# Kernel optimization log

Measured on AMD Instinct MI355X. Metric: run time of the kernel, lower is better.

The kernel has to match this reference:

```python
import jax, jax.numpy as jnp
import numpy as np

B, C, H, W, K = 64, 64, 32, 32, 1024  # C == dim_dict, K == size_dict
BETA = 0.25


def setup_inputs() -> dict:
    key = jax.random.key(0)
    k1, k2, k3 = jax.random.split(key, 3)
    return {
        "z_from_encoder": jax.random.normal(k1, (B, C, H, W), dtype=jnp.float32),
        "codebook": jax.random.normal(k2, (K, C), dtype=jnp.float32),
        "codebook_weight": jax.random.normal(k3, (K,), dtype=jnp.float32),
        "flg_train": 1,
    }


def reference(z_from_encoder, codebook, codebook_weight, flg_train):
    # NCHW -> NHWC, flatten to (N, D)
    z = jnp.transpose(z_from_encoder, (0, 2, 3, 1))
    zf = z.reshape(-1, z.shape[-1])                      # (N, D)
    # squared euclidean distances via expansion (N, K)
    d = (jnp.sum(zf ** 2, axis=1, keepdims=True)
         + jnp.sum(codebook ** 2, axis=1)
         - 2.0 * zf @ codebook.T)
    idx = jnp.argmin(d, axis=1)                          # (N,)
    # one-hot @ codebook == gather
    z_q = codebook[idx].reshape(z.shape)                 # (B, H, W, D)
    if flg_train:
        loss = (BETA * jnp.mean((jax.lax.stop_gradient(z_q) - z) ** 2)
                + jnp.mean((z_q - jax.lax.stop_gradient(z)) ** 2))
    else:
        loss = jnp.float32(0.0)
    # straight-through estimator
    z_q_st = z + jax.lax.stop_gradient(z_q - z)
    # codebook usage histogram -> perplexity
    n_tok = zf.shape[0]
    e_mean = jnp.zeros((codebook.shape[0],), z.dtype).at[idx].add(1.0) / n_tok
    perplexity = jnp.exp(-jnp.sum(e_mean * jnp.log(e_mean + 1e-10)))
    z_q_out = jnp.transpose(z_q_st, (0, 3, 1, 2))        # back to NCHW
    return z_q_out, loss, perplexity
```

## Files before the change

kernel.cpp:

```cpp
#include <hip/hip_runtime.h>


typedef __attribute__((ext_vector_type(8))) short short8;
typedef __attribute__((ext_vector_type(4))) float float4v;

#define NELEM 4194304

#define WS_CBF   0
#define WS_C2H   262144
#define WS_HIST  266240
#define WS_LOSS  270336
#define WS_IDX   270592

__device__ __forceinline__ unsigned bf16_rne(float x) {
    unsigned u = __float_as_uint(x);
    return (u + 0x7fffu + ((u >> 16) & 1u)) >> 16;
}


__global__ __launch_bounds__(256) void prep_kernel(
    const float* __restrict__ z, const float* __restrict__ cb,
    ushort* __restrict__ zs, ushort* __restrict__ cbf, float* __restrict__ c2h,
    int* __restrict__ hist, float* __restrict__ loss_part)
{
    __shared__ float s_c2[2][16];
    int tid  = threadIdx.x;
    int lane = tid & 63, wave = tid >> 6;
    int quad = lane >> 4, col = lane & 15;
    int bx   = blockIdx.x;

    if (bx < 1024) {
        int tokbase = bx * 64;
        int bb = tokbase >> 10, hwb = tokbase & 1023;
        const float* zb = z + bb * 65536 + hwb;
        int g  = wave;
        int gg = bx * 4 + g;
        int rel = g * 16 + col;
#pragma unroll
        for (int st = 0; st < 2; st++) {
            short8 h8, l8;
#pragma unroll
            for (int j = 0; j < 8; j++) {
                int d = st * 32 + quad * 8 + j;
                float x = zb[d * 1024 + rel];
                unsigned hb = bf16_rne(x);
                h8[j] = (short)hb;
                l8[j] = (short)bf16_rne(x - __uint_as_float(hb << 16));
            }
            int base = (((gg * 2 + st) * 4 + quad) * 2 + 0) * 16 + col;
            *(short8*)(zs + base * 8)             = h8;
            *(short8*)(zs + (base + 16) * 8)      = l8;
        }
        return;
    }
    if (bx >= 1088) {
        hist[(bx - 1088) * 256 + tid] = 0;
        if (bx == 1088 && tid < 64) loss_part[tid] = 0.f;
        return;
    }
    int c = bx - 1024, fid = wave;
    int st = fid & 1, split = fid >> 1;
    int code  = c * 16 + col;
    int dbase = st * 32 + quad * 8;
    const float* cp = cb + code * 64 + dbase;
    float4v v0 = *(const float4v*)cp;
    float4v v1 = *(const float4v*)(cp + 4);
    float xs[8] = {v0.x, v0.y, v0.z, v0.w, v1.x, v1.y, v1.z, v1.w};
    short8 frag;
    float ssq = 0.f;
#pragma unroll
    for (int j = 0; j < 8; j++) {
        float x = xs[j];
        ssq = fmaf(x, x, ssq);
        unsigned hb = bf16_rne(x);
        if (split == 0) frag[j] = (short)hb;
        else            frag[j] = (short)bf16_rne(x - __uint_as_float(hb << 16));
    }
    *(short8*)(cbf + ((c * 4 + fid) * 64 + lane) * 8) = frag;
    if (split == 0) {
        ssq += __shfl_xor(ssq, 16);
        ssq += __shfl_xor(ssq, 32);
        if (quad == 0) s_c2[st][col] = ssq;
    }
    __syncthreads();
    if (tid < 16) c2h[c * 16 + tid] = -0.5f * (s_c2[0][tid] + s_c2[1][tid]);
}

__global__ __launch_bounds__(256, 3) void argmin_kernel(
    const ushort* __restrict__ zs, const ushort* __restrict__ cbf,
    const float* __restrict__ c2h, int* __restrict__ idx_out, int* __restrict__ hist)
{
    __shared__ float s_ms[4][64];
    __shared__ int   s_mi[4][64];

    int tid  = threadIdx.x;
    int lane = tid & 63, wave = tid >> 6;
    int quad = lane >> 4, col = lane & 15;
    int bx   = blockIdx.x;
    int tokbase = bx * 64;

    short8 ah[4][2], al[4][2];
#pragma unroll
    for (int g = 0; g < 4; g++) {
        int gg = bx * 4 + g;
#pragma unroll
        for (int st = 0; st < 2; st++) {
            int base = (((gg * 2 + st) * 4 + quad) * 2 + 0) * 16 + col;
            ah[g][st] = *(const short8*)(zs + base * 8);
            al[g][st] = *(const short8*)(zs + (base + 16) * 8);
        }
    }

    float best[4][4]; int bidx[4][4];
#pragma unroll
    for (int g = 0; g < 4; g++)
#pragma unroll
        for (int r = 0; r < 4; r++) { best[g][r] = -1e38f; bidx[g][r] = 0; }

    int cbase = wave << 4;
    const ushort* cw = cbf + lane * 8;
    {
        const ushort* p0 = cw + cbase * 2048;
        short8 nb0 = *(const short8*)(p0 + 0);
        short8 nb1 = *(const short8*)(p0 + 512);
        short8 nb2 = *(const short8*)(p0 + 1024);
        short8 nb3 = *(const short8*)(p0 + 1536);
        float  nini = c2h[cbase * 16 + col];
        for (int cc = 0; cc < 16; cc++) {
            short8 bh0 = nb0, bh1 = nb1, bl0 = nb2, bl1 = nb3;
            float  ini = nini;
            if (cc < 15) {
                const ushort* np = cw + (cbase + cc + 1) * 2048;
                nb0 = *(const short8*)(np + 0);
                nb1 = *(const short8*)(np + 512);
                nb2 = *(const short8*)(np + 1024);
                nb3 = *(const short8*)(np + 1536);
                nini = c2h[(cbase + cc + 1) * 16 + col];
            }
            int code = (cbase + cc) * 16 + col;
#pragma unroll
            for (int g = 0; g < 4; g++) {
                float4v acc = {ini, ini, ini, ini};
                acc = __builtin_amdgcn_mfma_f32_16x16x32_bf16(ah[g][0], bh0, acc, 0, 0, 0);
                acc = __builtin_amdgcn_mfma_f32_16x16x32_bf16(ah[g][1], bh1, acc, 0, 0, 0);
                acc = __builtin_amdgcn_mfma_f32_16x16x32_bf16(ah[g][0], bl0, acc, 0, 0, 0);
                acc = __builtin_amdgcn_mfma_f32_16x16x32_bf16(ah[g][1], bl1, acc, 0, 0, 0);
                acc = __builtin_amdgcn_mfma_f32_16x16x32_bf16(al[g][0], bh0, acc, 0, 0, 0);
                acc = __builtin_amdgcn_mfma_f32_16x16x32_bf16(al[g][1], bh1, acc, 0, 0, 0);
#pragma unroll
                for (int r = 0; r < 4; r++) {
                    if (acc[r] > best[g][r]) { best[g][r] = acc[r]; bidx[g][r] = code; }
                }
            }
        }
    }

#pragma unroll
    for (int g = 0; g < 4; g++) {
#pragma unroll
        for (int r = 0; r < 4; r++) {
            float s = best[g][r]; int ix = bidx[g][r];
#pragma unroll
            for (int m = 1; m <= 8; m <<= 1) {
                float so = __shfl_xor(s, m);
                int   io = __shfl_xor(ix, m);
                if (so > s || (so == s && io < ix)) { s = so; ix = io; }
            }
            if (col == 0) {
                int t = g * 16 + quad * 4 + r;
                s_ms[wave][t] = s; s_mi[wave][t] = ix;
            }
        }
    }
    __syncthreads();

    if (tid < 64) {
        float sb = s_ms[0][tid]; int ib = s_mi[0][tid];
#pragma unroll
        for (int q = 1; q < 4; q++) {
            float sq_ = s_ms[q][tid];
            if (sq_ > sb) { sb = sq_; ib = s_mi[q][tid]; }
        }
        idx_out[tokbase + tid] = ib;
        atomicAdd(&hist[ib], 1);
    }
}

__global__ __launch_bounds__(256) void output_kernel(
    const float* __restrict__ z, const float* __restrict__ cb,
    const int* __restrict__ idx, float* __restrict__ out,
    float* __restrict__ loss_part)
{
    __shared__ int    s_row[128];
    __shared__ float4 s_q4[64 * 33];
    __shared__ float  s_red[4];

    int tid = threadIdx.x, bx = blockIdx.x;
    int tokbase = bx * 128;
    int bb = tokbase >> 10, hwb = tokbase & 1023;

    if (tid < 128) s_row[tid] = idx[tokbase + tid];
    __syncthreads();

#pragma unroll
    for (int p = 0; p < 32; p++) {
        int i = p * 256 + tid;
        int t = i >> 6, d = i & 63;
        float v = cb[s_row[t] * 64 + d];
        ((float*)s_q4)[(d * 33 + (t >> 2)) * 4 + (t & 3)] = v;
    }
    __syncthreads();

    const float* zb = z   + bb * 65536 + hwb;
    float*       ob = out + bb * 65536 + hwb;
    float ls = 0.f;
#pragma unroll
    for (int p = 0; p < 8; p++) {
        int fi = p * 256 + tid;
        int d = fi >> 5, tq = fi & 31;
        float4 zv = *(const float4*)(zb + d * 1024 + tq * 4);
        float4 qv = s_q4[d * 33 + tq];
        float d0 = qv.x - zv.x, d1 = qv.y - zv.y, d2 = qv.z - zv.z, d3 = qv.w - zv.w;
        float4 ov = {zv.x + d0, zv.y + d1, zv.z + d2, zv.w + d3};
        *(float4*)(ob + d * 1024 + tq * 4) = ov;
        ls += (d0 * d0 + d1 * d1) + (d2 * d2 + d3 * d3);
    }
#pragma unroll
    for (int off = 32; off; off >>= 1) ls += __shfl_down(ls, off);
    if ((tid & 63) == 0) s_red[tid >> 6] = ls;
    __syncthreads();
    if (tid == 0) {
        float v = (s_red[0] + s_red[1]) + (s_red[2] + s_red[3]);
        atomicAdd(&loss_part[bx & 63], v);
    }
}

__global__ __launch_bounds__(1024) void finalize_kernel(
    const int* __restrict__ hist, const float* __restrict__ loss_part,
    const int* __restrict__ flg, float* __restrict__ out) {
    __shared__ float red[16];
    int   k = threadIdx.x;
    float e = (float)hist[k] * (1.0f / 65536.0f);
    float v = e * logf(e + 1e-10f);
#pragma unroll
    for (int off = 32; off; off >>= 1) v += __shfl_down(v, off);
    if ((k & 63) == 0) red[k >> 6] = v;
    __syncthreads();
    if (k == 0) {
        float s = 0.f;
#pragma unroll
        for (int i = 0; i < 16; i++) s += red[i];
        out[NELEM + 1] = expf(-s);

        float ls = 0.f;
        for (int i = 0; i < 64; i++) ls += loss_part[i];
        float m    = ls * (1.0f / (float)NELEM);
        out[NELEM] = (*flg) ? (0.25f * m + m) : 0.0f;
    }
}

extern "C" void kernel_launch(void* const* d_in, const int* in_sizes, int n_in,
                              void* d_out, int out_size, void* d_ws, size_t ws_size,
                              hipStream_t stream) {
    const float* z   = (const float*)d_in[0];
    const float* cb  = (const float*)d_in[1];
    const int*   flg = (const int*)d_in[3];

    float* out = (float*)d_out;
    char*  ws  = (char*)d_ws;

    ushort* cbf       = (ushort*)(ws + WS_CBF);
    float*  c2h       = (float*)(ws + WS_C2H);
    int*    hist      = (int*)(ws + WS_HIST);
    float*  loss_part = (float*)(ws + WS_LOSS);
    int*    idx       = (int*)(ws + WS_IDX);
    ushort* zs        = (ushort*)d_out;

    prep_kernel<<<1092, 256, 0, stream>>>(z, cb, zs, cbf, c2h, hist, loss_part);
    argmin_kernel<<<1024, 256, 0, stream>>>(zs, cbf, c2h, idx, hist);
    output_kernel<<<512, 256, 0, stream>>>(z, cb, idx, out, loss_part);
    finalize_kernel<<<1, 1024, 0, stream>>>(hist, loss_part, flg, out);
}
```

Baseline: 135.6 us.

## Stage codebook chunks in LDS via async loads shared across waves

The argmin kernel is restructured. Each block now has 8 waves, each owning 16 tokens and sweeping all 64 codebook chunks. Before, each of 4 waves owned 64 tokens and a quarter of the codebook. Codebook fragments are double-buffered in LDS through global_load_lds by 4 waves and shared across all 8 waves, and c2h is cached in shared memory. This removes the cross-wave reduction and cuts per-wave register pressure. In exchange it adds a __syncthreads per chunk and does less MFMA work per B-fragment load.

```diff
diff --git a/kernel.cpp b/kernel.cpp
--- a/kernel.cpp
+++ b/kernel.cpp
@@ -15,6 +15,12 @@
 __device__ __forceinline__ unsigned bf16_rne(float x) {
     unsigned u = __float_as_uint(x);
     return (u + 0x7fffu + ((u >> 16) & 1u)) >> 16;
+}
+
+__device__ __forceinline__ void gl_lds16(const void* g, void* l) {
+    __builtin_amdgcn_global_load_lds(
+        (const __attribute__((address_space(1))) unsigned*)g,
+        (__attribute__((address_space(3))) unsigned*)l, 16, 0, 0);
 }
 
 
@@ -33,9 +39,8 @@
         int tokbase = bx * 64;
         int bb = tokbase >> 10, hwb = tokbase & 1023;
         const float* zb = z + bb * 65536 + hwb;
-        int g  = wave;
-        int gg = bx * 4 + g;
-        int rel = g * 16 + col;
+        int gg = bx * 4 + wave;
+        int rel = wave * 16 + col;
 #pragma unroll
         for (int st = 0; st < 2; st++) {
             short8 h8, l8;
@@ -48,8 +53,8 @@
                 l8[j] = (short)bf16_rne(x - __uint_as_float(hb << 16));
             }
             int base = (((gg * 2 + st) * 4 + quad) * 2 + 0) * 16 + col;
-            *(short8*)(zs + base * 8)             = h8;
-            *(short8*)(zs + (base + 16) * 8)      = l8;
+            *(short8*)(zs + base * 8)        = h8;
+            *(short8*)(zs + (base + 16) * 8) = l8;
         }
         return;
     }
@@ -86,103 +91,81 @@
     if (tid < 16) c2h[c * 16 + tid] = -0.5f * (s_c2[0][tid] + s_c2[1][tid]);
 }
 
-__global__ __launch_bounds__(256, 3) void argmin_kernel(
+__global__ __launch_bounds__(512, 4) void argmin_kernel(
     const ushort* __restrict__ zs, const ushort* __restrict__ cbf,
     const float* __restrict__ c2h, int* __restrict__ idx_out, int* __restrict__ hist)
 {
-    __shared__ float s_ms[4][64];
-    __shared__ int   s_mi[4][64];
+    __shared__ short8 s_b[2 * 4 * 64];
+    __shared__ float  s_c2h[1024];
 
     int tid  = threadIdx.x;
     int lane = tid & 63, wave = tid >> 6;
     int quad = lane >> 4, col = lane & 15;
     int bx   = blockIdx.x;
-    int tokbase = bx * 64;
-
-    short8 ah[4][2], al[4][2];
-#pragma unroll
-    for (int g = 0; g < 4; g++) {
-        int gg = bx * 4 + g;
-#pragma unroll
-        for (int st = 0; st < 2; st++) {
-            int base = (((gg * 2 + st) * 4 + quad) * 2 + 0) * 16 + col;
-            ah[g][st] = *(const short8*)(zs + base * 8);
-            al[g][st] = *(const short8*)(zs + (base + 16) * 8);
-        }
-    }
-
-    float best[4][4]; int bidx[4][4];
-#pragma unroll
-    for (int g = 0; g < 4; g++)
-#pragma unroll
-        for (int r = 0; r < 4; r++) { best[g][r] = -1e38f; bidx[g][r] = 0; }
-
-    int cbase = wave << 4;
-    const ushort* cw = cbf + lane * 8;
-    {
-        const ushort* p0 = cw + cbase * 2048;
-        short8 nb0 = *(const short8*)(p0 + 0);
-        short8 nb1 = *(const short8*)(p0 + 512);
-        short8 nb2 = *(const short8*)(p0 + 1024);
-        short8 nb3 = *(const short8*)(p0 + 1536);
-        float  nini = c2h[cbase * 16 + col];
-        for (int cc = 0; cc < 16; cc++) {
-            short8 bh0 = nb0, bh1 = nb1, bl0 = nb2, bl1 = nb3;
-            float  ini = nini;
-            if (cc < 15) {
-                const ushort* np = cw + (cbase + cc + 1) * 2048;
-                nb0 = *(const short8*)(np + 0);
-                nb1 = *(const short8*)(np + 512);
-                nb2 = *(const short8*)(np + 1024);
-                nb3 = *(const short8*)(np + 1536);
-                nini = c2h[(cbase + cc + 1) * 16 + col];
-            }
-            int code = (cbase + cc) * 16 + col;
-#pragma unroll
-            for (int g = 0; g < 4; g++) {
-                float4v acc = {ini, ini, ini, ini};
-                acc = __builtin_amdgcn_mfma_f32_16x16x32_bf16(ah[g][0], bh0, acc, 0, 0, 0);
-                acc = __builtin_amdgcn_mfma_f32_16x16x32_bf16(ah[g][1], bh1, acc, 0, 0, 0);
-                acc = __builtin_amdgcn_mfma_f32_16x16x32_bf16(ah[g][0], bl0, acc, 0, 0, 0);
-                acc = __builtin_amdgcn_mfma_f32_16x16x32_bf16(ah[g][1], bl1, acc, 0, 0, 0);
-                acc = __builtin_amdgcn_mfma_f32_16x16x32_bf16(al[g][0], bh0, acc, 0, 0, 0);
-                acc = __builtin_amdgcn_mfma_f32_16x16x32_bf16(al[g][1], bh1, acc, 0, 0, 0);
-#pragma unroll
-                for (int r = 0; r < 4; r++) {
-                    if (acc[r] > best[g][r]) { best[g][r] = acc[r]; bidx[g][r] = code; }
-                }
-            }
-        }
-    }
-
-#pragma unroll
-    for (int g = 0; g < 4; g++) {
+    const char* cbf_b = (const char*)cbf;
+
+    s_c2h[tid]       = c2h[tid];
+    s_c2h[tid + 512] = c2h[tid + 512];
+
+    int gg = bx * 8 + wave;
+    short8 ah[2], al[2];
+#pragma unroll
+    for (int st = 0; st < 2; st++) {
+        int base = (((gg * 2 + st) * 4 + quad) * 2 + 0) * 16 + col;
+        ah[st] = *(const short8*)(zs + base * 8);
+        al[st] = *(const short8*)(zs + (base + 16) * 8);
+    }
+
+    if (wave < 4)
+        gl_lds16(cbf_b + (0 * 4 + wave) * 1024 + lane * 16, &s_b[wave * 64]);
+    __syncthreads();
+
+    float best[4]; int bidx[4];
+#pragma unroll
+    for (int r = 0; r < 4; r++) { best[r] = -1e38f; bidx[r] = 0; }
+
+    for (int ch = 0; ch < 64; ch++) {
+        int buf = ch & 1;
+        if (ch < 63 && wave < 4)
+            gl_lds16(cbf_b + ((ch + 1) * 4 + wave) * 1024 + lane * 16,
+                     &s_b[((ch + 1) & 1) * 256 + wave * 64]);
+
+        const short8* bp = &s_b[buf * 256];
+        short8 bh0 = bp[0 * 64 + lane];
+        short8 bh1 = bp[1 * 64 + lane];
+        short8 bl0 = bp[2 * 64 + lane];
+        short8 bl1 = bp[3 * 64 + lane];
+        float  ini = s_c2h[ch * 16 + col];
+        int   code = ch * 16 + col;
+
+        float4v acc = {ini, ini, ini, ini};
+        acc = __builtin_amdgcn_mfma_f32_16x16x32_bf16(ah[0], bh0, acc, 0, 0, 0);
+        acc = __builtin_amdgcn_mfma_f32_16x16x32_bf16(ah[1], bh1, acc, 0, 0, 0);
+        acc = __builtin_amdgcn_mfma_f32_16x16x32_bf16(ah[0], bl0, acc, 0, 0, 0);
+        acc = __builtin_amdgcn_mfma_f32_16x16x32_bf16(ah[1], bl1, acc, 0, 0, 0);
+        acc = __builtin_amdgcn_mfma_f32_16x16x32_bf16(al[0], bh0, acc, 0, 0, 0);
+        acc = __builtin_amdgcn_mfma_f32_16x16x32_bf16(al[1], bh1, acc, 0, 0, 0);
 #pragma unroll
         for (int r = 0; r < 4; r++) {
-            float s = best[g][r]; int ix = bidx[g][r];
-#pragma unroll
-            for (int m = 1; m <= 8; m <<= 1) {
-                float so = __shfl_xor(s, m);
-                int   io = __shfl_xor(ix, m);
-                if (so > s || (so == s && io < ix)) { s = so; ix = io; }
-            }
-            if (col == 0) {
-                int t = g * 16 + quad * 4 + r;
-                s_ms[wave][t] = s; s_mi[wave][t] = ix;
-            }
-        }
-    }
-    __syncthreads();
-
-    if (tid < 64) {
-        float sb = s_ms[0][tid]; int ib = s_mi[0][tid];
-#pragma unroll
-        for (int q = 1; q < 4; q++) {
-            float sq_ = s_ms[q][tid];
-            if (sq_ > sb) { sb = sq_; ib = s_mi[q][tid]; }
-        }
-        idx_out[tokbase + tid] = ib;
-        atomicAdd(&hist[ib], 1);
+            if (acc[r] > best[r]) { best[r] = acc[r]; bidx[r] = code; }
+        }
+        __syncthreads();
+    }
+
+#pragma unroll
+    for (int r = 0; r < 4; r++) {
+        float s = best[r]; int ix = bidx[r];
+#pragma unroll
+        for (int m = 1; m <= 8; m <<= 1) {
+            float so = __shfl_xor(s, m);
+            int   io = __shfl_xor(ix, m);
+            if (so > s || (so == s && io < ix)) { s = so; ix = io; }
+        }
+        if (col == 0) {
+            int t = wave * 16 + quad * 4 + r;
+            idx_out[bx * 128 + t] = ix;
+            atomicAdd(&hist[ix], 1);
+        }
     }
 }
 
@@ -277,7 +260,7 @@
     ushort* zs        = (ushort*)d_out;
 
     prep_kernel<<<1092, 256, 0, stream>>>(z, cb, zs, cbf, c2h, hist, loss_part);
-    argmin_kernel<<<1024, 256, 0, stream>>>(zs, cbf, c2h, idx, hist);
+    argmin_kernel<<<512, 512, 0, stream>>>(zs, cbf, c2h, idx, hist);
     output_kernel<<<512, 256, 0, stream>>>(z, cb, idx, out, loss_part);
     finalize_kernel<<<1, 1024, 0, stream>>>(hist, loss_part, flg, out);
 }
```

New measurement: 156.9 us. 1.16x slower.
